# Performance work log

Measured on AMD Instinct MI355X. Metric: run time of the kernel, lower is better.

Reference implementation:

```python
import jax, jax.numpy as jnp
import numpy as np

N_NODES = 100000
N_EDGES = 3200000
D = 16
L = 3


def setup_inputs() -> dict:
    key = jax.random.key(0)
    ks = jax.random.split(key, 7)
    scale = 1.0 / np.sqrt(D)
    x = jax.random.normal(ks[0], (N_NODES, D), dtype=jnp.float32)
    edge_index = jax.random.randint(ks[1], (2, N_EDGES), 0, N_NODES, dtype=jnp.int64)
    Wl = jax.random.normal(ks[2], (L, D, D), dtype=jnp.float32) * scale
    bl = jax.random.normal(ks[3], (L, D), dtype=jnp.float32) * scale
    Wr = jax.random.normal(ks[4], (L, D, D), dtype=jnp.float32) * scale
    Wlin = jax.random.normal(ks[5], (L, D, D), dtype=jnp.float32) * scale
    blin = jax.random.normal(ks[6], (L, D), dtype=jnp.float32) * scale
    return {"x": x, "edge_index": edge_index, "Wl": Wl, "bl": bl,
            "Wr": Wr, "Wlin": Wlin, "blin": blin}


def reference(x, edge_index, Wl, bl, Wr, Wlin, blin):
    src = edge_index[0]
    dst = edge_index[1]
    n = x.shape[0]
    # in-degree for mean aggregation (PyG SAGEConv aggr='mean')
    deg = jax.ops.segment_sum(jnp.ones((src.shape[0],), dtype=x.dtype), dst,
                              num_segments=n)
    denom = jnp.maximum(deg, 1.0)[:, None]  # nodes with no in-edges -> 0 agg
    for i in range(Wl.shape[0]):
        # gather source features, scatter-mean onto targets
        agg = jax.ops.segment_sum(x[src], dst, num_segments=n) / denom
        conv = agg @ Wl[i].T + bl[i] + x @ Wr[i].T  # SAGEConv: lin_l(agg)+lin_r(x)
        x = conv + x @ Wlin[i].T + blin[i]          # + Linear residual
    return x
```

## Files before the change

kernel.cpp:

```cpp
#include <hip/hip_runtime.h>

#define N_NODES 100000
#define N_EDGES 3200000
#define D 16
#define L 3

#define TILE 128
#define NB ((N_NODES + TILE - 1) / TILE)
#define CAP 4608
#define NBLK 500
#define SEG (N_EDGES / NBLK)
#define BINT 1024
#define LT 512

__device__ __forceinline__ unsigned packbf(float a, float b) {
    unsigned ua = __float_as_uint(a); ua += 0x7FFFu + ((ua >> 16) & 1u);
    unsigned ub = __float_as_uint(b); ub += 0x7FFFu + ((ub >> 16) & 1u);
    return (ua >> 16) | (ub & 0xFFFF0000u);
}
#define BLO(u) __uint_as_float((u) << 16)
#define BHI(u) __uint_as_float((u) & 0xFFFF0000u)

__global__ void cvt_kernel(const float* __restrict__ x, unsigned* __restrict__ xbf, int n4) {
    int t = blockIdx.x * blockDim.x + threadIdx.x;
    if (t >= n4) return;
    float4 v = *(const float4*)(x + (size_t)t * 4);
    uint2 o; o.x = packbf(v.x, v.y); o.y = packbf(v.z, v.w);
    *(uint2*)(xbf + (size_t)t * 2) = o;
}

__global__ void bin_scatter(const int* __restrict__ src, const int* __restrict__ dst,
                            int* __restrict__ cursor, unsigned* __restrict__ ebuf, int E) {
    __shared__ int lcnt[NB];
    __shared__ int lbase[NB];
    for (int i = threadIdx.x; i < NB; i += BINT) lcnt[i] = 0;
    __syncthreads();
    int b0 = blockIdx.x * SEG, b1 = min(E, b0 + SEG);
    for (int e = b0 + threadIdx.x * 4; e < b1; e += BINT * 4) {
        int4 d4 = *(const int4*)(dst + e);
        atomicAdd(&lcnt[d4.x >> 7], 1);
        atomicAdd(&lcnt[d4.y >> 7], 1);
        atomicAdd(&lcnt[d4.z >> 7], 1);
        atomicAdd(&lcnt[d4.w >> 7], 1);
    }
    __syncthreads();
    for (int i = threadIdx.x; i < NB; i += BINT) {
        int v = lcnt[i];
        lbase[i] = v ? (i * CAP + atomicAdd(&cursor[i], v)) : 0;
    }
    __syncthreads();
    for (int i = threadIdx.x; i < NB; i += BINT) lcnt[i] = 0;
    __syncthreads();
    for (int e = b0 + threadIdx.x * 4; e < b1; e += BINT * 4) {
        int4 d4 = *(const int4*)(dst + e);
        int4 s4 = *(const int4*)(src + e);
        int b_, pos;
        b_ = d4.x >> 7; pos = lbase[b_] + atomicAdd(&lcnt[b_], 1);
        ebuf[pos] = ((unsigned)(d4.x & 127) << 17) | (unsigned)s4.x;
        b_ = d4.y >> 7; pos = lbase[b_] + atomicAdd(&lcnt[b_], 1);
        ebuf[pos] = ((unsigned)(d4.y & 127) << 17) | (unsigned)s4.y;
        b_ = d4.z >> 7; pos = lbase[b_] + atomicAdd(&lcnt[b_], 1);
        ebuf[pos] = ((unsigned)(d4.z & 127) << 17) | (unsigned)s4.z;
        b_ = d4.w >> 7; pos = lbase[b_] + atomicAdd(&lcnt[b_], 1);
        ebuf[pos] = ((unsigned)(d4.w & 127) << 17) | (unsigned)s4.w;
    }
}

__device__ __forceinline__ void agg_xform(
    const float* __restrict__ xin, const unsigned* __restrict__ xbf,
    const unsigned* se2, const int* lofs, int n_loc,
    const float* sWl, const float* sWc, const float* sbc,
    float* __restrict__ xout, unsigned* __restrict__ xbf_out,
    int emit_bf, int b, int N, int tid) {
    int q = tid & 3;
    int n = b * TILE + n_loc;
    if (n >= N) return;

    int s0 = lofs[n_loc];
    int s1 = lofs[n_loc + 1];
    int deg = s1 - s0;

    int lane2 = q >> 1;
    int ho = (q & 1) * 4;

    float acc[8] = {0.f,0.f,0.f,0.f,0.f,0.f,0.f,0.f};
    float bcc[8] = {0.f,0.f,0.f,0.f,0.f,0.f,0.f,0.f};
    int i = s0;
    for (; i + 8 <= s1; i += 8) {
        unsigned p0 = se2[i + 0 + lane2] & 0x1FFFF;
        unsigned p1 = se2[i + 2 + lane2] & 0x1FFFF;
        unsigned p2 = se2[i + 4 + lane2] & 0x1FFFF;
        unsigned p3 = se2[i + 6 + lane2] & 0x1FFFF;
        uint4 g0 = *(const uint4*)(xbf + (size_t)p0 * 8 + ho);
        uint4 g1 = *(const uint4*)(xbf + (size_t)p1 * 8 + ho);
        uint4 g2 = *(const uint4*)(xbf + (size_t)p2 * 8 + ho);
        uint4 g3 = *(const uint4*)(xbf + (size_t)p3 * 8 + ho);
        acc[0] += BLO(g0.x); acc[1] += BHI(g0.x); acc[2] += BLO(g0.y); acc[3] += BHI(g0.y);
        acc[4] += BLO(g0.z); acc[5] += BHI(g0.z); acc[6] += BLO(g0.w); acc[7] += BHI(g0.w);
        bcc[0] += BLO(g1.x); bcc[1] += BHI(g1.x); bcc[2] += BLO(g1.y); bcc[3] += BHI(g1.y);
        bcc[4] += BLO(g1.z); bcc[5] += BHI(g1.z); bcc[6] += BLO(g1.w); bcc[7] += BHI(g1.w);
        acc[0] += BLO(g2.x); acc[1] += BHI(g2.x); acc[2] += BLO(g2.y); acc[3] += BHI(g2.y);
        acc[4] += BLO(g2.z); acc[5] += BHI(g2.z); acc[6] += BLO(g2.w); acc[7] += BHI(g2.w);
        bcc[0] += BLO(g3.x); bcc[1] += BHI(g3.x); bcc[2] += BLO(g3.y); bcc[3] += BHI(g3.y);
        bcc[4] += BLO(g3.z); bcc[5] += BHI(g3.z); bcc[6] += BLO(g3.w); bcc[7] += BHI(g3.w);
    }
    for (; i + 2 <= s1; i += 2) {
        unsigned p = se2[i + lane2] & 0x1FFFF;
        uint4 g = *(const uint4*)(xbf + (size_t)p * 8 + ho);
        acc[0] += BLO(g.x); acc[1] += BHI(g.x); acc[2] += BLO(g.y); acc[3] += BHI(g.y);
        acc[4] += BLO(g.z); acc[5] += BHI(g.z); acc[6] += BLO(g.w); acc[7] += BHI(g.w);
    }
    if (i < s1 && lane2 == 0) {
        unsigned p = se2[i] & 0x1FFFF;
        uint4 g = *(const uint4*)(xbf + (size_t)p * 8 + ho);
        acc[0] += BLO(g.x); acc[1] += BHI(g.x); acc[2] += BLO(g.y); acc[3] += BHI(g.y);
        acc[4] += BLO(g.z); acc[5] += BHI(g.z); acc[6] += BLO(g.w); acc[7] += BHI(g.w);
    }
    #pragma unroll
    for (int k = 0; k < 8; k++) acc[k] += bcc[k];
    #pragma unroll
    for (int k = 0; k < 8; k++) acc[k] += __shfl_xor(acc[k], 2, 4);

    int srcAbs = (tid & 63 & ~3) | (q >> 1);
    float inv = 1.0f / fmaxf((float)deg, 1.0f);
    float a[4];
    #pragma unroll
    for (int k = 0; k < 4; k++) {
        float lo = __shfl(acc[k], srcAbs);
        float hi = __shfl(acc[4 + k], srcAbs);
        a[k] = ((q & 1) ? hi : lo) * inv;
    }

    float4 xq = *(const float4*)(xin + (size_t)n * D + q * 4);
    float xv[4] = { xq.x, xq.y, xq.z, xq.w };

    float o[4];
    #pragma unroll
    for (int j = 0; j < D; j++) {
        float p = 0.f;
        #pragma unroll
        for (int k = 0; k < 4; k++) {
            int kk = q * 4 + k;
            p += a[k] * sWl[j * D + kk] + xv[k] * sWc[j * D + kk];
        }
        p += __shfl_xor(p, 1, 4);
        p += __shfl_xor(p, 2, 4);
        if ((j >> 2) == q) o[j & 3] = p + sbc[j];
    }
    *(float4*)(xout + (size_t)n * D + q * 4) = make_float4(o[0], o[1], o[2], o[3]);
    if (emit_bf) {
        uint2 ob; ob.x = packbf(o[0], o[1]); ob.y = packbf(o[2], o[3]);
        *(uint2*)(xbf_out + (size_t)n * 8 + q * 2) = ob;
    }
}

__global__ void layer0_kernel(const float* __restrict__ xin, const unsigned* __restrict__ xbf,
                              unsigned* __restrict__ ebuf, const int* __restrict__ cnt,
                              int* __restrict__ node_start, int* __restrict__ gperm,
                              const float* __restrict__ Wl, const float* __restrict__ bl,
                              const float* __restrict__ Wr, const float* __restrict__ Wlin,
                              const float* __restrict__ blin,
                              float* __restrict__ xout, unsigned* __restrict__ xbf_out, int N) {
    __shared__ unsigned se[CAP];
    __shared__ unsigned se2[CAP];
    __shared__ int lcnt[TILE];
    __shared__ int sscan[TILE];
    __shared__ int lofs[TILE + 1];
    __shared__ int sdeg[TILE];
    __shared__ int perm[TILE];
    __shared__ float sWl[D * D];
    __shared__ float sWc[D * D];
    __shared__ float sbc[D];

    int tid = threadIdx.x;
    int b = blockIdx.x;
    int base = b * CAP;
    int nE = min(cnt[b], CAP);

    if (tid < D * D) { sWl[tid] = Wl[tid]; sWc[tid] = Wr[tid] + Wlin[tid]; }
    if (tid < D) sbc[tid] = bl[tid] + blin[tid];
    if (tid < TILE) lcnt[tid] = 0;
    __syncthreads();
    for (int i = tid; i < nE; i += LT) {
        unsigned p = ebuf[base + i];
        se[i] = p;
        atomicAdd(&lcnt[p >> 17], 1);
    }
    __syncthreads();
    if (tid < TILE) sscan[tid] = lcnt[tid];
    __syncthreads();
    for (int off = 1; off < TILE; off <<= 1) {
        int t = (tid < TILE && tid >= off) ? sscan[tid - off] : 0;
        __syncthreads();
        if (tid < TILE) sscan[tid] += t;
        __syncthreads();
    }
    if (tid < TILE) {
        int excl = sscan[tid] - lcnt[tid];
        lofs[tid] = excl;
        lcnt[tid] = excl;
        sdeg[tid] = sscan[tid] - excl;
        node_start[b * TILE + tid] = excl;
        if (tid == TILE - 1) lofs[TILE] = sscan[tid];
    }
    __syncthreads();
    if (tid < TILE) {
        int dm = sdeg[tid];
        int r = 0;
        for (int j = 0; j < TILE; j++) {
            int dj = sdeg[j];
            r += (dj > dm) || (dj == dm && j < tid);
        }
        perm[r] = tid;
        gperm[b * TILE + r] = tid;
    }
    for (int i = tid; i < nE; i += LT) {
        unsigned p = se[i];
        int pos = atomicAdd(&lcnt[p >> 17], 1);
        se2[pos] = p;
    }
    __syncthreads();
    for (int i = tid; i < nE; i += LT)
        ebuf[base + i] = se2[i];

    agg_xform(xin, xbf, se2, lofs, perm[tid >> 2], sWl, sWc, sbc,
              xout, xbf_out, 1, b, N, tid);
}

__global__ void layerN_kernel(const float* __restrict__ xin, const unsigned* __restrict__ xbf,
                              const unsigned* __restrict__ ebuf, const int* __restrict__ cnt,
                              const int* __restrict__ node_start, const int* __restrict__ gperm,
                              const float* __restrict__ Wl, const float* __restrict__ bl,
                              const float* __restrict__ Wr, const float* __restrict__ Wlin,
                              const float* __restrict__ blin,
                              float* __restrict__ xout, unsigned* __restrict__ xbf_out,
                              int emit_bf, int N) {
    __shared__ unsigned se2[CAP];
    __shared__ int lofs[TILE + 1];
    __shared__ float sWl[D * D];
    __shared__ float sWc[D * D];
    __shared__ float sbc[D];

    int tid = threadIdx.x;
    int b = blockIdx.x;
    int base = b * CAP;
    int nE = min(cnt[b], CAP);

    if (tid < D * D) { sWl[tid] = Wl[tid]; sWc[tid] = Wr[tid] + Wlin[tid]; }
    if (tid < D) sbc[tid] = bl[tid] + blin[tid];
    if (tid < TILE) lofs[tid] = node_start[b * TILE + tid];
    if (tid == 0) lofs[TILE] = nE;
    for (int i = tid; i < nE; i += LT) se2[i] = ebuf[base + i];
    int n_loc = gperm[b * TILE + (tid >> 2)];
    __syncthreads();

    agg_xform(xin, xbf, se2, lofs, n_loc, sWl, sWc, sbc,
              xout, xbf_out, emit_bf, b, N, tid);
}

extern "C" void kernel_launch(void* const* d_in, const int* in_sizes, int n_in,
                              void* d_out, int out_size, void* d_ws, size_t ws_size,
                              hipStream_t stream) {
    const float* x    = (const float*)d_in[0];
    const int*   ei   = (const int*)d_in[1];
    const float* Wl   = (const float*)d_in[2];
    const float* bl   = (const float*)d_in[3];
    const float* Wr   = (const float*)d_in[4];
    const float* Wlin = (const float*)d_in[5];
    const float* blin = (const float*)d_in[6];
    float* out = (float*)d_out;

    const int* src = ei;
    const int* dst = ei + N_EDGES;

    char* w = (char*)d_ws;
    unsigned* ebuf   = (unsigned*)w;  w += (size_t)NB * CAP * 4;
    float* bufA      = (float*)w;     w += (size_t)N_NODES * D * 4;
    float* bufB      = (float*)w;     w += (size_t)N_NODES * D * 4;
    unsigned* xbf0   = (unsigned*)w;  w += (size_t)N_NODES * 8 * 4;
    unsigned* xbf1   = (unsigned*)w;  w += (size_t)N_NODES * 8 * 4;
    int*   cursor    = (int*)w;       w += (size_t)NB * 4;
    int*   node_start= (int*)w;       w += (size_t)NB * TILE * 4;
    int*   gperm     = (int*)w;       w += (size_t)NB * TILE * 4;

    hipMemsetAsync(cursor, 0, (size_t)NB * 4, stream);
    cvt_kernel<<<(N_NODES * D / 4 + 255) / 256, 256, 0, stream>>>(x, xbf0, N_NODES * D / 4);
    bin_scatter<<<NBLK, BINT, 0, stream>>>(src, dst, cursor, ebuf, N_EDGES);

    layer0_kernel<<<NB, LT, 0, stream>>>(
        x, xbf0, ebuf, cursor, node_start, gperm,
        Wl, bl, Wr, Wlin, blin, bufA, xbf1, N_NODES);
    layerN_kernel<<<NB, LT, 0, stream>>>(
        bufA, xbf1, ebuf, cursor, node_start, gperm,
        Wl + D * D, bl + D, Wr + D * D, Wlin + D * D, blin + D, bufB, xbf0, 1, N_NODES);
    layerN_kernel<<<NB, LT, 0, stream>>>(
        bufB, xbf0, ebuf, cursor, node_start, gperm,
        Wl + 2 * D * D, bl + 2 * D, Wr + 2 * D * D, Wlin + 2 * D * D, blin + 2 * D,
        out, xbf1, 0, N_NODES);
}
```

Baseline: 209.5 us.

## Locally sort edges in shared memory before coalesced bucket writes; fold memset into cvt

The binning kernel now does a block-wide prefix scan over per-bucket counts, places each edge into a shared-memory array sorted by bucket, and then writes it out to the global edge buffer in index order, so consecutive threads write contiguous runs per bucket. Before, each edge was written straight to a scattered global location. The separate memset of the bucket cursors is folded into the conversion kernel to save one launch. In exchange the kernel needs about 25KB more shared memory per block for the sorted and bucket arrays, plus extra scan barriers.

Result: faster. 199.5 us (-4.8%).

```diff
diff --git a/kernel.cpp b/kernel.cpp
--- a/kernel.cpp
+++ b/kernel.cpp
@@ -21,8 +21,10 @@
 #define BLO(u) __uint_as_float((u) << 16)
 #define BHI(u) __uint_as_float((u) & 0xFFFF0000u)
 
-__global__ void cvt_kernel(const float* __restrict__ x, unsigned* __restrict__ xbf, int n4) {
+__global__ void cvt_kernel(const float* __restrict__ x, unsigned* __restrict__ xbf,
+                           int* __restrict__ cursor, int n4) {
     int t = blockIdx.x * blockDim.x + threadIdx.x;
+    if (t < NB) cursor[t] = 0;
     if (t >= n4) return;
     float4 v = *(const float4*)(x + (size_t)t * 4);
     uint2 o; o.x = packbf(v.x, v.y); o.y = packbf(v.z, v.w);
@@ -32,11 +34,15 @@
 __global__ void bin_scatter(const int* __restrict__ src, const int* __restrict__ dst,
                             int* __restrict__ cursor, unsigned* __restrict__ ebuf, int E) {
     __shared__ int lcnt[NB];
-    __shared__ int lbase[NB];
-    for (int i = threadIdx.x; i < NB; i += BINT) lcnt[i] = 0;
+    __shared__ int ldiff[NB];
+    __shared__ int lofs[NB];
+    __shared__ unsigned sorted[SEG];
+    __shared__ unsigned short sbkt[SEG];
+    int tid = threadIdx.x;
+    for (int i = tid; i < NB; i += BINT) lcnt[i] = 0;
     __syncthreads();
     int b0 = blockIdx.x * SEG, b1 = min(E, b0 + SEG);
-    for (int e = b0 + threadIdx.x * 4; e < b1; e += BINT * 4) {
+    for (int e = b0 + tid * 4; e < b1; e += BINT * 4) {
         int4 d4 = *(const int4*)(dst + e);
         atomicAdd(&lcnt[d4.x >> 7], 1);
         atomicAdd(&lcnt[d4.y >> 7], 1);
@@ -44,25 +50,44 @@
         atomicAdd(&lcnt[d4.w >> 7], 1);
     }
     __syncthreads();
-    for (int i = threadIdx.x; i < NB; i += BINT) {
-        int v = lcnt[i];
-        lbase[i] = v ? (i * CAP + atomicAdd(&cursor[i], v)) : 0;
-    }
-    __syncthreads();
-    for (int i = threadIdx.x; i < NB; i += BINT) lcnt[i] = 0;
-    __syncthreads();
-    for (int e = b0 + threadIdx.x * 4; e < b1; e += BINT * 4) {
+    {
+        int v = (tid < NB) ? lcnt[tid] : 0;
+        sorted[tid] = (unsigned)v;
+        __syncthreads();
+        for (int off = 1; off < BINT; off <<= 1) {
+            unsigned t = (tid >= off) ? sorted[tid - off] : 0u;
+            __syncthreads();
+            sorted[tid] += t;
+            __syncthreads();
+        }
+        if (tid < NB) {
+            int incl = (int)sorted[tid];
+            int excl = incl - v;
+            lofs[tid] = excl;
+            int g = v ? (tid * CAP + atomicAdd(&cursor[tid], v)) : 0;
+            ldiff[tid] = g - excl;
+            lcnt[tid] = excl;
+        }
+        __syncthreads();
+    }
+    for (int e = b0 + tid * 4; e < b1; e += BINT * 4) {
         int4 d4 = *(const int4*)(dst + e);
         int4 s4 = *(const int4*)(src + e);
         int b_, pos;
-        b_ = d4.x >> 7; pos = lbase[b_] + atomicAdd(&lcnt[b_], 1);
-        ebuf[pos] = ((unsigned)(d4.x & 127) << 17) | (unsigned)s4.x;
-        b_ = d4.y >> 7; pos = lbase[b_] + atomicAdd(&lcnt[b_], 1);
-        ebuf[pos] = ((unsigned)(d4.y & 127) << 17) | (unsigned)s4.y;
-        b_ = d4.z >> 7; pos = lbase[b_] + atomicAdd(&lcnt[b_], 1);
-        ebuf[pos] = ((unsigned)(d4.z & 127) << 17) | (unsigned)s4.z;
-        b_ = d4.w >> 7; pos = lbase[b_] + atomicAdd(&lcnt[b_], 1);
-        ebuf[pos] = ((unsigned)(d4.w & 127) << 17) | (unsigned)s4.w;
+        b_ = d4.x >> 7; pos = atomicAdd(&lcnt[b_], 1);
+        sorted[pos] = ((unsigned)(d4.x & 127) << 17) | (unsigned)s4.x; sbkt[pos] = (unsigned short)b_;
+        b_ = d4.y >> 7; pos = atomicAdd(&lcnt[b_], 1);
+        sorted[pos] = ((unsigned)(d4.y & 127) << 17) | (unsigned)s4.y; sbkt[pos] = (unsigned short)b_;
+        b_ = d4.z >> 7; pos = atomicAdd(&lcnt[b_], 1);
+        sorted[pos] = ((unsigned)(d4.z & 127) << 17) | (unsigned)s4.z; sbkt[pos] = (unsigned short)b_;
+        b_ = d4.w >> 7; pos = atomicAdd(&lcnt[b_], 1);
+        sorted[pos] = ((unsigned)(d4.w & 127) << 17) | (unsigned)s4.w; sbkt[pos] = (unsigned short)b_;
+    }
+    __syncthreads();
+    int nLoc = b1 - b0;
+    for (int i = tid; i < nLoc; i += BINT) {
+        int b_ = sbkt[i];
+        ebuf[ldiff[b_] + i] = sorted[i];
     }
 }
 
@@ -283,8 +308,8 @@
     int*   node_start= (int*)w;       w += (size_t)NB * TILE * 4;
     int*   gperm     = (int*)w;       w += (size_t)NB * TILE * 4;
 
-    hipMemsetAsync(cursor, 0, (size_t)NB * 4, stream);
-    cvt_kernel<<<(N_NODES * D / 4 + 255) / 256, 256, 0, stream>>>(x, xbf0, N_NODES * D / 4);
+    cvt_kernel<<<(N_NODES * D / 4 + 255) / 256, 256, 0, stream>>>(
+        x, xbf0, cursor, N_NODES * D / 4);
     bin_scatter<<<NBLK, BINT, 0, stream>>>(src, dst, cursor, ebuf, N_EDGES);
 
     layer0_kernel<<<NB, LT, 0, stream>>>(
```
